# Kernel optimization log

Measured on AMD Instinct MI355X. Metric: run time of the kernel, lower is better.

Reference implementation:

```python
import jax, jax.numpy as jnp
import numpy as np

N_NODES = 50000
N_GRAPHS = 250
NODES_PER_GRAPH = 200
EDGES_PER_GRAPH = 3200  # avg degree 16
F_IN = 128
EMB = 128
HID = 128
VOCAB = 1000
N_REL = 8


def setup_inputs() -> dict:
    key = jax.random.key(0)
    ks = jax.random.split(key, 16)

    # message: col 0 = discrete token id (stored as float), col 1 = continuous value
    disc = jax.random.randint(ks[0], (N_GRAPHS,), 0, VOCAB).astype(jnp.float32)
    cont = jax.random.normal(ks[1], (N_GRAPHS,), dtype=jnp.float32)
    message = jnp.stack([disc, cont], axis=1)  # [B, 2]

    x = jax.random.normal(ks[2], (N_NODES, F_IN), dtype=jnp.float32)

    # within-graph edges: local indices + per-graph node offset
    offs = (jnp.arange(N_GRAPHS, dtype=jnp.int64) * NODES_PER_GRAPH)[:, None]
    src = (jax.random.randint(ks[3], (N_GRAPHS, EDGES_PER_GRAPH), 0, NODES_PER_GRAPH) + offs).reshape(-1)
    dst = (jax.random.randint(ks[4], (N_GRAPHS, EDGES_PER_GRAPH), 0, NODES_PER_GRAPH) + offs).reshape(-1)
    edge_index = jnp.stack([src, dst], axis=0).astype(jnp.int64)  # [2, E]
    edge_type = jax.random.randint(ks[5], (N_GRAPHS * EDGES_PER_GRAPH,), 0, N_REL).astype(jnp.int64)

    batch = jnp.repeat(jnp.arange(N_GRAPHS, dtype=jnp.int64), NODES_PER_GRAPH)  # [N]

    s = 0.05
    W1 = jax.random.normal(ks[6], (N_REL, F_IN, EMB), dtype=jnp.float32) * s
    root1 = jax.random.normal(ks[7], (F_IN, EMB), dtype=jnp.float32) * s
    b1 = jnp.zeros((EMB,), dtype=jnp.float32)
    W2 = jax.random.normal(ks[8], (N_REL, EMB, EMB), dtype=jnp.float32) * s
    root2 = jax.random.normal(ks[9], (EMB, EMB), dtype=jnp.float32) * s
    b2 = jnp.zeros((EMB,), dtype=jnp.float32)
    embed_table = jax.random.normal(ks[10], (VOCAB, EMB), dtype=jnp.float32) * s
    cont_w = jax.random.normal(ks[11], (1, EMB), dtype=jnp.float32) * s
    cont_b = jnp.zeros((EMB,), dtype=jnp.float32)
    msg_w = jax.random.normal(ks[12], (2 * EMB, HID), dtype=jnp.float32) * s
    msg_b = jnp.zeros((HID,), dtype=jnp.float32)

    return {
        "message": message, "x": x, "edge_index": edge_index, "edge_type": edge_type,
        "batch": batch, "max_nodes": NODES_PER_GRAPH,
        "W1": W1, "root1": root1, "b1": b1, "W2": W2, "root2": root2, "b2": b2,
        "embed_table": embed_table, "cont_w": cont_w, "cont_b": cont_b,
        "msg_w": msg_w, "msg_b": msg_b,
    }


def _rgcn_conv(h, src, dst, edge_type, W, root, b, n_nodes, n_rel):
    # per-node per-relation transform, then gather per edge: avoids [E,F,F] weight gather
    hW = jnp.einsum('nf,rfo->nro', h, W)          # [N, R, O]
    msg = hW[src, edge_type]                       # [E, O]
    # mean aggregation per (dst, relation) as in PyG RGCNConv(aggr='mean')
    key_dr = dst * n_rel + edge_type
    cnt = jax.ops.segment_sum(jnp.ones_like(edge_type, dtype=h.dtype), key_dr,
                              num_segments=n_nodes * n_rel)
    norm = 1.0 / jnp.maximum(cnt[key_dr], 1.0)     # [E]
    agg = jax.ops.segment_sum(msg * norm[:, None], dst, num_segments=n_nodes)  # [N, O]
    return agg + h @ root + b


def reference(message, x, edge_index, edge_type, batch, max_nodes,
              W1, root1, b1, W2, root2, b2,
              embed_table, cont_w, cont_b, msg_w, msg_b):
    n_nodes = x.shape[0]
    n_rel = W1.shape[0]
    n_graphs = message.shape[0]
    src, dst = edge_index[0], edge_index[1]

    # --- RGCN node embeddings (2 layers, ReLU between) ---
    h = _rgcn_conv(x, src, dst, edge_type, W1, root1, b1, n_nodes, n_rel)
    h = jax.nn.relu(h)
    node_emb = _rgcn_conv(h, src, dst, edge_type, W2, root2, b2, n_nodes, n_rel)  # [N, EMB]

    # --- message representation ---
    disc_tok = message[:, 0].astype(jnp.int32)
    disc_emb = embed_table[disc_tok]                                   # [B, EMB]
    cont_emb = jax.nn.relu(message[:, 1:2] @ cont_w + cont_b)          # [B, EMB]
    combined = jnp.concatenate([disc_emb, cont_emb], axis=1)           # [B, 2*EMB]
    message_repr = jax.nn.relu(combined @ msg_w + msg_b)               # [B, HID]

    # --- per-node dot score against its graph's message, padded per graph ---
    scores = jnp.einsum('ne,ne->n', node_emb, message_repr[batch])     # [N]
    counts = jax.ops.segment_sum(jnp.ones((n_nodes,), dtype=jnp.int32), batch,
                                 num_segments=n_graphs)
    start = jnp.cumsum(counts) - counts                                # exclusive cumsum
    pos = jnp.arange(n_nodes) - start[batch]                           # slot within graph
    logits = jnp.full((n_graphs, max_nodes), -jnp.inf, dtype=scores.dtype)
    logits = logits.at[batch, pos].set(scores)
    return logits
```

## Files before the change

### kernel.cpp

```cpp
#include <hip/hip_runtime.h>
#include <stdint.h>

#define G_   250
#define P_   200
#define EPG  3200
#define E_   800000
#define F_   128
#define R_   8
#define HROW 136
#define NKEY (R_ * P_)
#define BSTG (8 * 4 * 64 * 8)

typedef _Float16 f16x8 __attribute__((ext_vector_type(8)));
typedef _Float16 f16x4 __attribute__((ext_vector_type(4)));
typedef float    f32x4 __attribute__((ext_vector_type(4)));
typedef float    f32x16 __attribute__((ext_vector_type(16)));

__global__ __launch_bounds__(256) void k_wstage(const float* __restrict__ W1, const float* __restrict__ root1,
                                                const float* __restrict__ W2, const float* __restrict__ root2,
                                                _Float16* __restrict__ wf) {
  int t = blockIdx.x * 256 + threadIdx.x;
  int n = t & 127;
  int k = (t >> 7) & 127;
  int rl_ = t >> 14;
  int r = rl_ % 9, l = rl_ / 9;
  const float* Wl = (l == 0) ? W1 : W2;
  const float* rt = (l == 0) ? root1 : root2;
  float v = (r < 8) ? Wl[(r * F_ + k) * F_ + n] : rt[k * F_ + n];
  int lane = (n & 31) | (((k >> 3) & 1) << 5);
  int j = k & 7, kt = k >> 4, ntj = n >> 5;
  wf[((((l * 9 + r) * 8 + kt) * 4 + ntj) * 64 + lane) * 8 + j] = (_Float16)v;
}

__global__ __launch_bounds__(512, 1) void k_main(
    const float* __restrict__ x, const int* __restrict__ ei, const int* __restrict__ et,
    const _Float16* __restrict__ wf, const float* __restrict__ b1, const float* __restrict__ b2,
    const float* __restrict__ message, const float* __restrict__ embed,
    const float* __restrict__ cw, const float* __restrict__ cb,
    const float* __restrict__ mw, const float* __restrict__ mb,
    float* __restrict__ out) {
  __shared__ __attribute__((aligned(16))) _Float16 hbuf0[P_ * HROW];
  __shared__ __attribute__((aligned(16))) _Float16 hbuf1[P_ * HROW];
  __shared__ __attribute__((aligned(16))) _Float16 Bstage[BSTG];
  __shared__ unsigned short csrS[EPG];
  __shared__ int offsS[NKEY + 1];
  __shared__ float msgS[F_ + 1];

  int g = blockIdx.x, tid = threadIdx.x;
  int lane = tid & 63, wave = tid >> 6;
  int m32 = lane & 31, kh = lane >> 5;

  int*   Sint = (int*)hbuf1;
  int*   cnt  = Sint;
  int*   cur  = Sint + 1600;
  int*   eRec = Sint + 3200;
  float* comb = (float*)(Sint + 6400);
  float* red  = (float*)(Sint + 6656);

  for (int i = tid; i < P_ * 32; i += 512) {
    int row = i >> 5, c4 = i & 31;
    const float4 v = ((const float4*)x)[(g * P_ + row) * 32 + c4];
    f16x4 pk = { (_Float16)v.x, (_Float16)v.y, (_Float16)v.z, (_Float16)v.w };
    *((f16x4*)&hbuf0[row * HROW + c4 * 4]) = pk;
  }
  for (int i = tid; i < NKEY; i += 512) { cnt[i] = 0; cur[i] = 0; }
  if (tid < F_) {
    int tok = (int)message[g * 2];
    float cont = message[g * 2 + 1];
    comb[tid] = embed[tok * F_ + tid];
    float ce = cont * cw[tid] + cb[tid];
    comb[F_ + tid] = ce > 0.0f ? ce : 0.0f;
  }
  __syncthreads();

  int base = g * EPG, nbase = g * P_;
  if (wave < 6) {
    for (int e = wave * 64 + lane; e < EPG; e += 384) {
      int s = ei[base + e] - nbase;
      int d = ei[E_ + base + e] - nbase;
      int r = et[base + e];
      eRec[e] = s | (d << 8) | (r << 16);
      atomicAdd(&cnt[r * P_ + d], 1);
    }
  } else {
    int col = tid & 127;
    float acc = 0.0f;
#pragma unroll 16
    for (int k2 = 0; k2 < 256; k2++) acc += comb[k2] * mw[k2 * F_ + col];
    red[col] = acc;
  }
  __syncthreads();

  if (wave == 0) {
    int4 vv[8];
    int osum = 0;
    if (lane < 50) {
      const int4* cp = (const int4*)(cnt + lane * 32);
#pragma unroll
      for (int i = 0; i < 8; i++) { vv[i] = cp[i]; osum += vv[i].x + vv[i].y + vv[i].z + vv[i].w; }
    }
    int incl = osum;
#pragma unroll
    for (int d = 1; d < 64; d <<= 1) {
      int t2 = __shfl_up(incl, d, 64);
      if (lane >= d) incl += t2;
    }
    int run = incl - osum;
    if (lane < 50) {
#pragma unroll
      for (int i = 0; i < 8; i++) {
        offsS[lane * 32 + i * 4 + 0] = run; run += vv[i].x;
        offsS[lane * 32 + i * 4 + 1] = run; run += vv[i].y;
        offsS[lane * 32 + i * 4 + 2] = run; run += vv[i].z;
        offsS[lane * 32 + i * 4 + 3] = run; run += vv[i].w;
      }
    }
    if (lane == 0) offsS[NKEY] = EPG;
  } else if (wave == 1) {
    float m0 = mb[lane] + red[lane];
    float m1 = mb[lane + 64] + red[lane + 64];
    m0 = m0 > 0.0f ? m0 : 0.0f;
    m1 = m1 > 0.0f ? m1 : 0.0f;
    msgS[lane] = m0; msgS[lane + 64] = m1;
    float p = m0 * b2[lane] + m1 * b2[lane + 64];
#pragma unroll
    for (int d = 32; d > 0; d >>= 1) p += __shfl_xor(p, d, 64);
    if (lane == 0) msgS[F_] = p;
  }
  __syncthreads();

  for (int e = tid; e < EPG; e += 512) {
    int rec = eRec[e];
    int s = rec & 255, d = (rec >> 8) & 255, r = rec >> 16;
    int key = r * P_ + d;
    int pos = atomicAdd(&cur[key], 1);
    csrS[offsS[key] + pos] = (unsigned short)s;
  }
  __syncthreads();

  int jobBase = wave * 25;
  bool rowAct = (m32 < 25);
  int myD = jobBase + m32;
  int ck = kh * 8;

  for (int l = 0; l < 2; l++) {
    const _Float16* Ap = (l == 0) ? hbuf0 : hbuf1;
    f32x16 acc[4];
#pragma unroll
    for (int nt = 0; nt < 4; nt++)
#pragma unroll
      for (int i = 0; i < 16; i++) acc[nt][i] = 0.0f;
    const _Float16* wl = wf + l * (9 * BSTG);
    for (int r = 0; r < 9; r++) {
      const _Float16* wr = wl + r * BSTG;
      f16x8 st[4];
#pragma unroll
      for (int i = 0; i < 4; i++)
        st[i] = *((const f16x8*)(wr + i * 4096 + tid * 8));
      f16x8 a[8];
      if (r < 8) {
        int o = 0, n = 0;
        if (rowAct) { int key = r * P_ + myD; o = offsS[key]; n = offsS[key + 1] - o; }
        f16x8 z = {0, 0, 0, 0, 0, 0, 0, 0};
#pragma unroll
        for (int kt = 0; kt < 8; kt++) a[kt] = z;
        int t = 0;
        for (; t + 2 <= n; t += 2) {
          int s0 = (int)csrS[o + t];
          int s1 = (int)csrS[o + t + 1];
          const _Float16* hp0 = &Ap[s0 * HROW + ck];
          const _Float16* hp1 = &Ap[s1 * HROW + ck];
          f16x8 u0[8], u1[8];
#pragma unroll
          for (int kt = 0; kt < 8; kt++) u0[kt] = *((const f16x8*)(hp0 + kt * 16));
#pragma unroll
          for (int kt = 0; kt < 8; kt++) u1[kt] = *((const f16x8*)(hp1 + kt * 16));
#pragma unroll
          for (int kt = 0; kt < 8; kt++) a[kt] += u0[kt] + u1[kt];
        }
        if (t < n) {
          int s0 = (int)csrS[o + t];
          const _Float16* hp0 = &Ap[s0 * HROW + ck];
#pragma unroll
          for (int kt = 0; kt < 8; kt++) a[kt] += *((const f16x8*)(hp0 + kt * 16));
        }
        float nf = (n > 0) ? 1.0f / (float)n : 0.0f;
        _Float16 nh = (_Float16)nf;
#pragma unroll
        for (int kt = 0; kt < 8; kt++) a[kt] *= nh;
      } else {
        int rowA = jobBase + (rowAct ? m32 : 24);
        const _Float16* hp = &Ap[rowA * HROW + ck];
#pragma unroll
        for (int kt = 0; kt < 8; kt++) a[kt] = *((const f16x8*)(hp + kt * 16));
      }
#pragma unroll
      for (int i = 0; i < 4; i++)
        *((f16x8*)(Bstage + i * 4096 + tid * 8)) = st[i];
      __syncthreads();
#pragma unroll
      for (int nt = 0; nt < 4; nt++) {
#pragma unroll
        for (int kt = 0; kt < 8; kt++) {
          f16x8 b = *((const f16x8*)&Bstage[((kt * 4 + nt) * 64 + lane) * 8]);
          acc[nt] = __builtin_amdgcn_mfma_f32_32x32x16_f16(a[kt], b, acc[nt], 0, 0, 0);
        }
      }
      __syncthreads();
    }
    if (l == 0) {
#pragma unroll
      for (int nt = 0; nt < 4; nt++) {
        int col = nt * 32 + m32;
        float bias = b1[col];
#pragma unroll
        for (int reg = 0; reg < 16; reg++) {
          int row = (reg & 3) + 8 * (reg >> 2) + 4 * kh;
          if (row < 25) {
            float v = acc[nt][reg] + bias;
            v = v > 0.0f ? v : 0.0f;
            hbuf1[(jobBase + row) * HROW + col] = (_Float16)v;
          }
        }
      }
      __syncthreads();
    } else {
      float db2 = msgS[F_];
#pragma unroll
      for (int reg = 0; reg < 16; reg++) {
        int row = (reg & 3) + 8 * (reg >> 2) + 4 * kh;
        float p = 0.0f;
#pragma unroll
        for (int nt = 0; nt < 4; nt++)
          p += acc[nt][reg] * msgS[nt * 32 + m32];
        p += __shfl_xor(p, 16, 32);
        p += __shfl_xor(p, 8, 32);
        p += __shfl_xor(p, 4, 32);
        p += __shfl_xor(p, 2, 32);
        p += __shfl_xor(p, 1, 32);
        if (m32 == 0 && row < 25)
          out[g * P_ + jobBase + row] = p + db2;
      }
    }
  }
}

extern "C" void kernel_launch(void* const* d_in, const int* in_sizes, int n_in,
                              void* d_out, int out_size, void* d_ws, size_t ws_size,
                              hipStream_t stream) {
  const float* message = (const float*)d_in[0];
  const float* x       = (const float*)d_in[1];
  const int*   ei      = (const int*)d_in[2];
  const int*   et      = (const int*)d_in[3];
  const float* W1      = (const float*)d_in[6];
  const float* root1   = (const float*)d_in[7];
  const float* b1      = (const float*)d_in[8];
  const float* W2      = (const float*)d_in[9];
  const float* root2   = (const float*)d_in[10];
  const float* b2      = (const float*)d_in[11];
  const float* embed   = (const float*)d_in[12];
  const float* cw      = (const float*)d_in[13];
  const float* cb      = (const float*)d_in[14];
  const float* mw      = (const float*)d_in[15];
  const float* mb      = (const float*)d_in[16];

  _Float16* wfrag = (_Float16*)d_ws;
  float*    out   = (float*)d_out;

  hipLaunchKernelGGL(k_wstage, dim3(1152), dim3(256), 0, stream, W1, root1, W2, root2, wfrag);
  hipLaunchKernelGGL(k_main, dim3(G_), dim3(512), 0, stream, x, ei, et, wfrag, b1, b2,
                     message, embed, cw, cb, mw, mb, out);
}
```

Before: 173.4 us.

## Halve block to 4 waves, each computing two 32-row tiles with register-held weights

The main kernel drops from 8 to 4 waves per graph block. Each wave now handles 50 destination rows as two MFMA row tiles, and the weight fragments are loaded straight from global memory into registers instead of through a shared staging buffer. This removes the two per-relation block barriers and the LDS stage, and reuses each B fragment across two tiles. The cost is much higher register pressure (64 accumulators plus 32 B fragments plus A), with a risk of spills, and fewer waves left to hide gather latency. The weight pre-staging kernel also now writes coalesced output in fragment order.

```diff
diff --git a/kernel.cpp b/kernel.cpp
--- a/kernel.cpp
+++ b/kernel.cpp
@@ -20,19 +20,56 @@
                                                 const float* __restrict__ W2, const float* __restrict__ root2,
                                                 _Float16* __restrict__ wf) {
   int t = blockIdx.x * 256 + threadIdx.x;
-  int n = t & 127;
-  int k = (t >> 7) & 127;
-  int rl_ = t >> 14;
+  int j    = t & 7;
+  int lane = (t >> 3) & 63;
+  int ntj  = (t >> 9) & 3;
+  int kt   = (t >> 11) & 7;
+  int rl_  = t >> 14;
   int r = rl_ % 9, l = rl_ / 9;
   const float* Wl = (l == 0) ? W1 : W2;
   const float* rt = (l == 0) ? root1 : root2;
+  int k = kt * 16 + (lane >> 5) * 8 + j;
+  int n = ntj * 32 + (lane & 31);
   float v = (r < 8) ? Wl[(r * F_ + k) * F_ + n] : rt[k * F_ + n];
-  int lane = (n & 31) | (((k >> 3) & 1) << 5);
-  int j = k & 7, kt = k >> 4, ntj = n >> 5;
-  wf[((((l * 9 + r) * 8 + kt) * 4 + ntj) * 64 + lane) * 8 + j] = (_Float16)v;
+  wf[t] = (_Float16)v;
 }
 
-__global__ __launch_bounds__(512, 1) void k_main(
+__device__ __forceinline__ void gather_agg(const _Float16* __restrict__ Ap,
+                                           const unsigned short* __restrict__ csr,
+                                           const int* __restrict__ offs,
+                                           int key, int act, int ck, f16x8* a) {
+  int o = 0, n = 0;
+  if (act) { o = offs[key]; n = offs[key + 1] - o; }
+  f16x8 z = {0, 0, 0, 0, 0, 0, 0, 0};
+#pragma unroll
+  for (int kt = 0; kt < 8; kt++) a[kt] = z;
+  int t = 0;
+  for (; t + 2 <= n; t += 2) {
+    int s0 = (int)csr[o + t];
+    int s1 = (int)csr[o + t + 1];
+    const _Float16* hp0 = &Ap[s0 * HROW + ck];
+    const _Float16* hp1 = &Ap[s1 * HROW + ck];
+    f16x8 u0[8], u1[8];
+#pragma unroll
+    for (int kt = 0; kt < 8; kt++) u0[kt] = *((const f16x8*)(hp0 + kt * 16));
+#pragma unroll
+    for (int kt = 0; kt < 8; kt++) u1[kt] = *((const f16x8*)(hp1 + kt * 16));
+#pragma unroll
+    for (int kt = 0; kt < 8; kt++) a[kt] += u0[kt] + u1[kt];
+  }
+  if (t < n) {
+    int s0 = (int)csr[o + t];
+    const _Float16* hp0 = &Ap[s0 * HROW + ck];
+#pragma unroll
+    for (int kt = 0; kt < 8; kt++) a[kt] += *((const f16x8*)(hp0 + kt * 16));
+  }
+  float nf = (n > 0) ? 1.0f / (float)n : 0.0f;
+  _Float16 nh = (_Float16)nf;
+#pragma unroll
+  for (int kt = 0; kt < 8; kt++) a[kt] *= nh;
+}
+
+__global__ __launch_bounds__(256, 1) void k_main(
     const float* __restrict__ x, const int* __restrict__ ei, const int* __restrict__ et,
     const _Float16* __restrict__ wf, const float* __restrict__ b1, const float* __restrict__ b2,
     const float* __restrict__ message, const float* __restrict__ embed,
@@ -41,7 +78,6 @@
     float* __restrict__ out) {
   __shared__ __attribute__((aligned(16))) _Float16 hbuf0[P_ * HROW];
   __shared__ __attribute__((aligned(16))) _Float16 hbuf1[P_ * HROW];
-  __shared__ __attribute__((aligned(16))) _Float16 Bstage[BSTG];
   __shared__ unsigned short csrS[EPG];
   __shared__ int offsS[NKEY + 1];
   __shared__ float msgS[F_ + 1];
@@ -57,13 +93,13 @@
   float* comb = (float*)(Sint + 6400);
   float* red  = (float*)(Sint + 6656);
 
-  for (int i = tid; i < P_ * 32; i += 512) {
+  for (int i = tid; i < P_ * 32; i += 256) {
     int row = i >> 5, c4 = i & 31;
     const float4 v = ((const float4*)x)[(g * P_ + row) * 32 + c4];
     f16x4 pk = { (_Float16)v.x, (_Float16)v.y, (_Float16)v.z, (_Float16)v.w };
     *((f16x4*)&hbuf0[row * HROW + c4 * 4]) = pk;
   }
-  for (int i = tid; i < NKEY; i += 512) { cnt[i] = 0; cur[i] = 0; }
+  for (int i = tid; i < NKEY; i += 256) { cnt[i] = 0; cur[i] = 0; }
   if (tid < F_) {
     int tok = (int)message[g * 2];
     float cont = message[g * 2 + 1];
@@ -74,8 +110,8 @@
   __syncthreads();
 
   int base = g * EPG, nbase = g * P_;
-  if (wave < 6) {
-    for (int e = wave * 64 + lane; e < EPG; e += 384) {
+  if (wave < 3) {
+    for (int e = wave * 64 + lane; e < EPG; e += 192) {
       int s = ei[base + e] - nbase;
       int d = ei[E_ + base + e] - nbase;
       int r = et[base + e];
@@ -83,11 +119,14 @@
       atomicAdd(&cnt[r * P_ + d], 1);
     }
   } else {
-    int col = tid & 127;
-    float acc = 0.0f;
-#pragma unroll 16
-    for (int k2 = 0; k2 < 256; k2++) acc += comb[k2] * mw[k2 * F_ + col];
-    red[col] = acc;
+    float a0 = 0.0f, a1 = 0.0f;
+#pragma unroll 8
+    for (int k2 = 0; k2 < 256; k2++) {
+      float c = comb[k2];
+      a0 += c * mw[k2 * F_ + lane];
+      a1 += c * mw[k2 * F_ + lane + 64];
+    }
+    red[lane] = a0; red[lane + 64] = a1;
   }
   __syncthreads();
 
@@ -129,7 +168,7 @@
   }
   __syncthreads();
 
-  for (int e = tid; e < EPG; e += 512) {
+  for (int e = tid; e < EPG; e += 256) {
     int rec = eRec[e];
     int s = rec & 255, d = (rec >> 8) & 255, r = rec >> 16;
     int key = r * P_ + d;
@@ -138,75 +177,48 @@
   }
   __syncthreads();
 
-  int jobBase = wave * 25;
-  bool rowAct = (m32 < 25);
-  int myD = jobBase + m32;
+  int jobBase = wave * 50;
   int ck = kh * 8;
+  int actB = (m32 < 18);
 
   for (int l = 0; l < 2; l++) {
     const _Float16* Ap = (l == 0) ? hbuf0 : hbuf1;
-    f32x16 acc[4];
+    f32x16 accA[4], accB[4];
 #pragma unroll
     for (int nt = 0; nt < 4; nt++)
 #pragma unroll
-      for (int i = 0; i < 16; i++) acc[nt][i] = 0.0f;
+      for (int i = 0; i < 16; i++) { accA[nt][i] = 0.0f; accB[nt][i] = 0.0f; }
     const _Float16* wl = wf + l * (9 * BSTG);
     for (int r = 0; r < 9; r++) {
       const _Float16* wr = wl + r * BSTG;
-      f16x8 st[4];
-#pragma unroll
-      for (int i = 0; i < 4; i++)
-        st[i] = *((const f16x8*)(wr + i * 4096 + tid * 8));
-      f16x8 a[8];
+      f16x8 bf[8][4];
+#pragma unroll
+      for (int kt = 0; kt < 8; kt++)
+#pragma unroll
+        for (int nt = 0; nt < 4; nt++)
+          bf[kt][nt] = *((const f16x8*)(wr + ((kt * 4 + nt) * 64 + lane) * 8));
+      f16x8 aA[8], aB[8];
       if (r < 8) {
-        int o = 0, n = 0;
-        if (rowAct) { int key = r * P_ + myD; o = offsS[key]; n = offsS[key + 1] - o; }
-        f16x8 z = {0, 0, 0, 0, 0, 0, 0, 0};
-#pragma unroll
-        for (int kt = 0; kt < 8; kt++) a[kt] = z;
-        int t = 0;
-        for (; t + 2 <= n; t += 2) {
-          int s0 = (int)csrS[o + t];
-          int s1 = (int)csrS[o + t + 1];
-          const _Float16* hp0 = &Ap[s0 * HROW + ck];
-          const _Float16* hp1 = &Ap[s1 * HROW + ck];
-          f16x8 u0[8], u1[8];
-#pragma unroll
-          for (int kt = 0; kt < 8; kt++) u0[kt] = *((const f16x8*)(hp0 + kt * 16));
-#pragma unroll
-          for (int kt = 0; kt < 8; kt++) u1[kt] = *((const f16x8*)(hp1 + kt * 16));
-#pragma unroll
-          for (int kt = 0; kt < 8; kt++) a[kt] += u0[kt] + u1[kt];
+        gather_agg(Ap, csrS, offsS, r * P_ + jobBase + m32, 1, ck, aA);
+        gather_agg(Ap, csrS, offsS, r * P_ + jobBase + 32 + m32, actB, ck, aB);
+      } else {
+        int rowA = jobBase + m32;
+        int rowB = jobBase + 32 + (actB ? m32 : 17);
+        const _Float16* hpA = &Ap[rowA * HROW + ck];
+        const _Float16* hpB = &Ap[rowB * HROW + ck];
+#pragma unroll
+        for (int kt = 0; kt < 8; kt++) aA[kt] = *((const f16x8*)(hpA + kt * 16));
+#pragma unroll
+        for (int kt = 0; kt < 8; kt++) aB[kt] = *((const f16x8*)(hpB + kt * 16));
+      }
+#pragma unroll
+      for (int kt = 0; kt < 8; kt++) {
+#pragma unroll
+        for (int nt = 0; nt < 4; nt++) {
+          accA[nt] = __builtin_amdgcn_mfma_f32_32x32x16_f16(aA[kt], bf[kt][nt], accA[nt], 0, 0, 0);
+          accB[nt] = __builtin_amdgcn_mfma_f32_32x32x16_f16(aB[kt], bf[kt][nt], accB[nt], 0, 0, 0);
         }
-        if (t < n) {
-          int s0 = (int)csrS[o + t];
-          const _Float16* hp0 = &Ap[s0 * HROW + ck];
-#pragma unroll
-          for (int kt = 0; kt < 8; kt++) a[kt] += *((const f16x8*)(hp0 + kt * 16));
-        }
-        float nf = (n > 0) ? 1.0f / (float)n : 0.0f;
-        _Float16 nh = (_Float16)nf;
-#pragma unroll
-        for (int kt = 0; kt < 8; kt++) a[kt] *= nh;
-      } else {
-        int rowA = jobBase + (rowAct ? m32 : 24);
-        const _Float16* hp = &Ap[rowA * HROW + ck];
-#pragma unroll
-        for (int kt = 0; kt < 8; kt++) a[kt] = *((const f16x8*)(hp + kt * 16));
-      }
-#pragma unroll
-      for (int i = 0; i < 4; i++)
-        *((f16x8*)(Bstage + i * 4096 + tid * 8)) = st[i];
-      __syncthreads();
-#pragma unroll
-      for (int nt = 0; nt < 4; nt++) {
-#pragma unroll
-        for (int kt = 0; kt < 8; kt++) {
-          f16x8 b = *((const f16x8*)&Bstage[((kt * 4 + nt) * 64 + lane) * 8]);
-          acc[nt] = __builtin_amdgcn_mfma_f32_32x32x16_f16(a[kt], b, acc[nt], 0, 0, 0);
-        }
-      }
-      __syncthreads();
+      }
     }
     if (l == 0) {
 #pragma unroll
@@ -216,30 +228,45 @@
 #pragma unroll
         for (int reg = 0; reg < 16; reg++) {
           int row = (reg & 3) + 8 * (reg >> 2) + 4 * kh;
-          if (row < 25) {
-            float v = acc[nt][reg] + bias;
-            v = v > 0.0f ? v : 0.0f;
-            hbuf1[(jobBase + row) * HROW + col] = (_Float16)v;
+          float vA = accA[nt][reg] + bias;
+          vA = vA > 0.0f ? vA : 0.0f;
+          hbuf1[(jobBase + row) * HROW + col] = (_Float16)vA;
+          if (row < 18) {
+            float vB = accB[nt][reg] + bias;
+            vB = vB > 0.0f ? vB : 0.0f;
+            hbuf1[(jobBase + 32 + row) * HROW + col] = (_Float16)vB;
           }
         }
       }
       __syncthreads();
     } else {
       float db2 = msgS[F_];
+      float mg[4];
+#pragma unroll
+      for (int nt = 0; nt < 4; nt++) mg[nt] = msgS[nt * 32 + m32];
 #pragma unroll
       for (int reg = 0; reg < 16; reg++) {
         int row = (reg & 3) + 8 * (reg >> 2) + 4 * kh;
-        float p = 0.0f;
-#pragma unroll
-        for (int nt = 0; nt < 4; nt++)
-          p += acc[nt][reg] * msgS[nt * 32 + m32];
-        p += __shfl_xor(p, 16, 32);
-        p += __shfl_xor(p, 8, 32);
-        p += __shfl_xor(p, 4, 32);
-        p += __shfl_xor(p, 2, 32);
-        p += __shfl_xor(p, 1, 32);
-        if (m32 == 0 && row < 25)
-          out[g * P_ + jobBase + row] = p + db2;
+        float pA = 0.0f, pB = 0.0f;
+#pragma unroll
+        for (int nt = 0; nt < 4; nt++) {
+          pA += accA[nt][reg] * mg[nt];
+          pB += accB[nt][reg] * mg[nt];
+        }
+        pA += __shfl_xor(pA, 16, 32);
+        pA += __shfl_xor(pA, 8, 32);
+        pA += __shfl_xor(pA, 4, 32);
+        pA += __shfl_xor(pA, 2, 32);
+        pA += __shfl_xor(pA, 1, 32);
+        pB += __shfl_xor(pB, 16, 32);
+        pB += __shfl_xor(pB, 8, 32);
+        pB += __shfl_xor(pB, 4, 32);
+        pB += __shfl_xor(pB, 2, 32);
+        pB += __shfl_xor(pB, 1, 32);
+        if (m32 == 0) {
+          out[g * P_ + jobBase + row] = pA + db2;
+          if (row < 18) out[g * P_ + jobBase + 32 + row] = pB + db2;
+        }
       }
     }
   }
@@ -268,6 +295,6 @@
   float*    out   = (float*)d_out;
 
   hipLaunchKernelGGL(k_wstage, dim3(1152), dim3(256), 0, stream, W1, root1, W2, root2, wfrag);
-  hipLaunchKernelGGL(k_main, dim3(G_), dim3(512), 0, stream, x, ei, et, wfrag, b1, b2,
+  hipLaunchKernelGGL(k_main, dim3(G_), dim3(256), 0, stream, x, ei, et, wfrag, b1, b2,
                      message, embed, cw, cb, mw, mb, out);
 }
```

After: 190.5 us. 9.9% more time.

## Double-buffer weight staging in LDS and prefetch next relation's weights

Applied to the files above, without the earlier changes.

Each relation's weight tile is now loaded from global memory one stage ahead. It is written into an alternating LDS buffer: the spare activation buffer of the other layer. This removes one of the two block barriers per relation and lets the global weight loads overlap the neighbour gather and the MFMA work. The first tile is preloaded during the input staging. The weight-staging kernel is rewritten so its writes are coalesced and its reads are strided. The added prefetch registers raise register pressure, and the scheme depends on the spare activation buffer being free at the right times.

```diff
diff --git a/kernel.cpp b/kernel.cpp
--- a/kernel.cpp
+++ b/kernel.cpp
@@ -20,16 +20,18 @@
                                                 const float* __restrict__ W2, const float* __restrict__ root2,
                                                 _Float16* __restrict__ wf) {
   int t = blockIdx.x * 256 + threadIdx.x;
-  int n = t & 127;
-  int k = (t >> 7) & 127;
-  int rl_ = t >> 14;
+  int j    = t & 7;
+  int lane = (t >> 3) & 63;
+  int ntj  = (t >> 9) & 3;
+  int kt   = (t >> 11) & 7;
+  int rl_  = t >> 14;
   int r = rl_ % 9, l = rl_ / 9;
   const float* Wl = (l == 0) ? W1 : W2;
   const float* rt = (l == 0) ? root1 : root2;
+  int k = kt * 16 + (lane >> 5) * 8 + j;
+  int n = ntj * 32 + (lane & 31);
   float v = (r < 8) ? Wl[(r * F_ + k) * F_ + n] : rt[k * F_ + n];
-  int lane = (n & 31) | (((k >> 3) & 1) << 5);
-  int j = k & 7, kt = k >> 4, ntj = n >> 5;
-  wf[((((l * 9 + r) * 8 + kt) * 4 + ntj) * 64 + lane) * 8 + j] = (_Float16)v;
+  wf[t] = (_Float16)v;
 }
 
 __global__ __launch_bounds__(512, 1) void k_main(
@@ -57,6 +59,11 @@
   float* comb = (float*)(Sint + 6400);
   float* red  = (float*)(Sint + 6656);
 
+  f16x8 st0[4];
+#pragma unroll
+  for (int i = 0; i < 4; i++)
+    st0[i] = *((const f16x8*)(wf + i * 4096 + tid * 8));
+
   for (int i = tid; i < P_ * 32; i += 512) {
     int row = i >> 5, c4 = i & 31;
     const float4 v = ((const float4*)x)[(g * P_ + row) * 32 + c4];
@@ -71,6 +78,9 @@
     float ce = cont * cw[tid] + cb[tid];
     comb[F_ + tid] = ce > 0.0f ? ce : 0.0f;
   }
+#pragma unroll
+  for (int i = 0; i < 4; i++)
+    *((f16x8*)(Bstage + i * 4096 + tid * 8)) = st0[i];
   __syncthreads();
 
   int base = g * EPG, nbase = g * P_;
@@ -145,6 +155,7 @@
 
   for (int l = 0; l < 2; l++) {
     const _Float16* Ap = (l == 0) ? hbuf0 : hbuf1;
+    _Float16* balt = (l == 0) ? hbuf1 : hbuf0;
     f32x16 acc[4];
 #pragma unroll
     for (int nt = 0; nt < 4; nt++)
@@ -152,11 +163,14 @@
       for (int i = 0; i < 16; i++) acc[nt][i] = 0.0f;
     const _Float16* wl = wf + l * (9 * BSTG);
     for (int r = 0; r < 9; r++) {
-      const _Float16* wr = wl + r * BSTG;
-      f16x8 st[4];
-#pragma unroll
-      for (int i = 0; i < 4; i++)
-        st[i] = *((const f16x8*)(wr + i * 4096 + tid * 8));
+      f16x8 st2[4];
+      bool haveNext = (r < 8) || (l == 0);
+      if (haveNext) {
+        const _Float16* wnext = (r < 8) ? (wl + (r + 1) * BSTG) : (wf + 9 * BSTG);
+#pragma unroll
+        for (int i = 0; i < 4; i++)
+          st2[i] = *((const f16x8*)(wnext + i * 4096 + tid * 8));
+      }
       f16x8 a[8];
       if (r < 8) {
         int o = 0, n = 0;
@@ -194,19 +208,27 @@
 #pragma unroll
         for (int kt = 0; kt < 8; kt++) a[kt] = *((const f16x8*)(hp + kt * 16));
       }
-#pragma unroll
-      for (int i = 0; i < 4; i++)
-        *((f16x8*)(Bstage + i * 4096 + tid * 8)) = st[i];
-      __syncthreads();
-#pragma unroll
-      for (int nt = 0; nt < 4; nt++) {
-#pragma unroll
-        for (int kt = 0; kt < 8; kt++) {
-          f16x8 b = *((const f16x8*)&Bstage[((kt * 4 + nt) * 64 + lane) * 8]);
+      const _Float16* bp = (r & 1) ? balt : Bstage;
+#pragma unroll
+      for (int kt = 0; kt < 8; kt++) {
+#pragma unroll
+        for (int nt = 0; nt < 4; nt++) {
+          f16x8 b = *((const f16x8*)&bp[((kt * 4 + nt) * 64 + lane) * 8]);
           acc[nt] = __builtin_amdgcn_mfma_f32_32x32x16_f16(a[kt], b, acc[nt], 0, 0, 0);
         }
       }
-      __syncthreads();
+      if (r < 8) {
+        _Float16* dst = ((r + 1) & 1) ? balt : Bstage;
+#pragma unroll
+        for (int i = 0; i < 4; i++)
+          *((f16x8*)(dst + i * 4096 + tid * 8)) = st2[i];
+        __syncthreads();
+      } else if (l == 0) {
+        __syncthreads();
+#pragma unroll
+        for (int i = 0; i < 4; i++)
+          *((f16x8*)(Bstage + i * 4096 + tid * 8)) = st2[i];
+      }
     }
     if (l == 0) {
 #pragma unroll
```

New measurement: 172.3 us. Within noise of the previous version (-0.6%).

## Load MFMA B fragments directly from global, drop LDS weight staging

Applied to the files above, without the earlier changes.

Each wave now reads its MFMA B-operand fragments straight from the pre-swizzled fp16 weight buffer in global/L2, in two halves. This removes the shared-memory Bstage buffer and the two block-wide barriers per relation. The freed LDS and a launch bound of two blocks per CU are meant to let two graphs share a CU. The weight staging kernel is also rewritten to write its output contiguously. In exchange every wave fetches all weights itself, raising L2 traffic and register pressure, and the wider launch bound may force register spills.

```diff
diff --git a/kernel.cpp b/kernel.cpp
--- a/kernel.cpp
+++ b/kernel.cpp
@@ -20,19 +20,21 @@
                                                 const float* __restrict__ W2, const float* __restrict__ root2,
                                                 _Float16* __restrict__ wf) {
   int t = blockIdx.x * 256 + threadIdx.x;
-  int n = t & 127;
-  int k = (t >> 7) & 127;
-  int rl_ = t >> 14;
+  int j    = t & 7;
+  int lane = (t >> 3) & 63;
+  int ntj  = (t >> 9) & 3;
+  int kt   = (t >> 11) & 7;
+  int rl_  = t >> 14;
   int r = rl_ % 9, l = rl_ / 9;
   const float* Wl = (l == 0) ? W1 : W2;
   const float* rt = (l == 0) ? root1 : root2;
+  int k = kt * 16 + (lane >> 5) * 8 + j;
+  int n = ntj * 32 + (lane & 31);
   float v = (r < 8) ? Wl[(r * F_ + k) * F_ + n] : rt[k * F_ + n];
-  int lane = (n & 31) | (((k >> 3) & 1) << 5);
-  int j = k & 7, kt = k >> 4, ntj = n >> 5;
-  wf[((((l * 9 + r) * 8 + kt) * 4 + ntj) * 64 + lane) * 8 + j] = (_Float16)v;
+  wf[t] = (_Float16)v;
 }
 
-__global__ __launch_bounds__(512, 1) void k_main(
+__global__ __launch_bounds__(512, 2) void k_main(
     const float* __restrict__ x, const int* __restrict__ ei, const int* __restrict__ et,
     const _Float16* __restrict__ wf, const float* __restrict__ b1, const float* __restrict__ b2,
     const float* __restrict__ message, const float* __restrict__ embed,
@@ -41,7 +43,6 @@
     float* __restrict__ out) {
   __shared__ __attribute__((aligned(16))) _Float16 hbuf0[P_ * HROW];
   __shared__ __attribute__((aligned(16))) _Float16 hbuf1[P_ * HROW];
-  __shared__ __attribute__((aligned(16))) _Float16 Bstage[BSTG];
   __shared__ unsigned short csrS[EPG];
   __shared__ int offsS[NKEY + 1];
   __shared__ float msgS[F_ + 1];
@@ -153,10 +154,12 @@
     const _Float16* wl = wf + l * (9 * BSTG);
     for (int r = 0; r < 9; r++) {
       const _Float16* wr = wl + r * BSTG;
-      f16x8 st[4];
-#pragma unroll
-      for (int i = 0; i < 4; i++)
-        st[i] = *((const f16x8*)(wr + i * 4096 + tid * 8));
+      f16x8 bA[4][4];
+#pragma unroll
+      for (int kt = 0; kt < 4; kt++)
+#pragma unroll
+        for (int nt = 0; nt < 4; nt++)
+          bA[kt][nt] = *((const f16x8*)(wr + ((kt * 4 + nt) * 64 + lane) * 8));
       f16x8 a[8];
       if (r < 8) {
         int o = 0, n = 0;
@@ -194,19 +197,22 @@
 #pragma unroll
         for (int kt = 0; kt < 8; kt++) a[kt] = *((const f16x8*)(hp + kt * 16));
       }
-#pragma unroll
-      for (int i = 0; i < 4; i++)
-        *((f16x8*)(Bstage + i * 4096 + tid * 8)) = st[i];
-      __syncthreads();
-#pragma unroll
-      for (int nt = 0; nt < 4; nt++) {
-#pragma unroll
-        for (int kt = 0; kt < 8; kt++) {
-          f16x8 b = *((const f16x8*)&Bstage[((kt * 4 + nt) * 64 + lane) * 8]);
-          acc[nt] = __builtin_amdgcn_mfma_f32_32x32x16_f16(a[kt], b, acc[nt], 0, 0, 0);
-        }
-      }
-      __syncthreads();
+      f16x8 bB[4][4];
+#pragma unroll
+      for (int kt = 0; kt < 4; kt++)
+#pragma unroll
+        for (int nt = 0; nt < 4; nt++)
+          bB[kt][nt] = *((const f16x8*)(wr + (((kt + 4) * 4 + nt) * 64 + lane) * 8));
+#pragma unroll
+      for (int kt = 0; kt < 4; kt++)
+#pragma unroll
+        for (int nt = 0; nt < 4; nt++)
+          acc[nt] = __builtin_amdgcn_mfma_f32_32x32x16_f16(a[kt], bA[kt][nt], acc[nt], 0, 0, 0);
+#pragma unroll
+      for (int kt = 0; kt < 4; kt++)
+#pragma unroll
+        for (int nt = 0; nt < 4; nt++)
+          acc[nt] = __builtin_amdgcn_mfma_f32_32x32x16_f16(a[kt + 4], bB[kt][nt], acc[nt], 0, 0, 0);
     }
     if (l == 0) {
 #pragma unroll
```

Measured after the change: 180.6 us. +4.2%, slower.
